# Optimization experiments

Hardware: AMD Instinct MI355X
Metric: run time of the kernel (lower is better)

## Reference

```python
import jax, jax.numpy as jnp
import numpy as np

NEG_SLOPE = 0.2  # PyG GATConv default negative_slope


def gat_conv(x, src, dst, W, a_src, a_dst, b):
    """PyG GATConv with concat=False (mean over heads). src/dst include self-loops."""
    N = x.shape[0]
    H, C = a_src.shape
    h = (x @ W).reshape(N, H, C)                      # [N,H,C]
    alpha_src = (h * a_src).sum(-1)                   # [N,H]
    alpha_dst = (h * a_dst).sum(-1)                   # [N,H]
    e = jax.nn.leaky_relu(alpha_src[src] + alpha_dst[dst], NEG_SLOPE)  # [E,H]
    # segment softmax over incoming edges of each dst node
    emax = jax.ops.segment_max(e, dst, num_segments=N)                 # [N,H]
    ex = jnp.exp(e - emax[dst])                                        # [E,H]
    denom = jax.ops.segment_sum(ex, dst, num_segments=N)               # [N,H]
    alpha = ex / denom[dst]                                            # [E,H]
    msg = h[src] * alpha[:, :, None]                                   # [E,H,C]
    out = jax.ops.segment_sum(msg, dst, num_segments=N)                # [N,H,C]
    return out.mean(axis=1) + b                                        # concat=False -> mean heads


def setup_inputs() -> dict:
    key = jax.random.key(0)
    ks = jax.random.split(key, 16)
    N, F_IN, H, C, E = 50000, 3, 4, 64, 800000
    inp = {
        "x": jax.random.normal(ks[0], (N, F_IN), dtype=jnp.float32),
        "edge_index": jax.random.randint(ks[1], (2, E), 0, N, dtype=jnp.int32),
        "W1": jax.random.normal(ks[2], (F_IN, H * C), dtype=jnp.float32) * 0.1,
        "a1_src": jax.random.normal(ks[3], (H, C), dtype=jnp.float32) * 0.1,
        "a1_dst": jax.random.normal(ks[4], (H, C), dtype=jnp.float32) * 0.1,
        "b1": jnp.zeros((C,), dtype=jnp.float32),
        "W2": jax.random.normal(ks[5], (C, H * C), dtype=jnp.float32) * 0.1,
        "a2_src": jax.random.normal(ks[6], (H, C), dtype=jnp.float32) * 0.1,
        "a2_dst": jax.random.normal(ks[7], (H, C), dtype=jnp.float32) * 0.1,
        "b2": jnp.zeros((C,), dtype=jnp.float32),
        "W3": jax.random.normal(ks[8], (C, H * C), dtype=jnp.float32) * 0.1,
        "a3_src": jax.random.normal(ks[9], (H, C), dtype=jnp.float32) * 0.1,
        "a3_dst": jax.random.normal(ks[10], (H, C), dtype=jnp.float32) * 0.1,
        "b3": jnp.zeros((C,), dtype=jnp.float32),
        "lin_w": jax.random.normal(ks[11], (C, 1), dtype=jnp.float32) * 0.1,
        "lin_b": jnp.zeros((1,), dtype=jnp.float32),
    }
    return inp


def reference(x, edge_index, W1, a1_src, a1_dst, b1, W2, a2_src, a2_dst, b2,
              W3, a3_src, a3_dst, b3, lin_w, lin_b):
    N = x.shape[0]
    loops = jnp.arange(N, dtype=edge_index.dtype)  # PyG add_self_loops=True default
    src = jnp.concatenate([edge_index[0], loops])
    dst = jnp.concatenate([edge_index[1], loops])

    h1 = jax.nn.elu(gat_conv(x, src, dst, W1, a1_src, a1_dst, b1))
    h2 = jax.nn.elu(gat_conv(h1, src, dst, W2, a2_src, a2_dst, b2)) + h1
    h3 = jax.nn.elu(gat_conv(h2, src, dst, W3, a3_src, a3_dst, b3)) + h2
    return h3 @ lin_w + lin_b
```

## Files before the change

kernel.cpp:

```cpp
#include <hip/hip_runtime.h>
#include <math.h>

#define HEADS 4
#define CH 64
#define HC 256

typedef __attribute__((ext_vector_type(8))) short bf16x8;
typedef __attribute__((ext_vector_type(4))) float f32x4;

__device__ __forceinline__ float lrelu(float v) { return v > 0.f ? v : 0.2f * v; }

__device__ __forceinline__ unsigned int f2bf(float f) {
    unsigned int u = __float_as_uint(f);
    u += 0x7fffu + ((u >> 16) & 1u);
    return u >> 16;
}
__device__ __forceinline__ float bf2f(unsigned short u) {
    return __uint_as_float(((unsigned int)u) << 16);
}

__device__ __forceinline__ float4 wave_sum4(float4 v) {
#pragma unroll
    for (int m = 32; m; m >>= 1) {
        v.x += __shfl_xor(v.x, m);
        v.y += __shfl_xor(v.y, m);
        v.z += __shfl_xor(v.z, m);
        v.w += __shfl_xor(v.w, m);
    }
    return v;
}

__global__ void count_kernel(const int* __restrict__ dst, int E, int vec_ok,
                             float scale8, int* __restrict__ deg,
                             int* __restrict__ slot) {
    int r = blockIdx.x & 7;
    int i = (blockIdx.x >> 3) * blockDim.x + threadIdx.x;
    int e0 = i * 4;
    if (e0 >= E) return;
    int d[4];
    int cnt;
    if (vec_ok && e0 + 3 < E) {
        int4 v = *(const int4*)(dst + e0);
        d[0] = v.x; d[1] = v.y; d[2] = v.z; d[3] = v.w; cnt = 4;
    } else {
        cnt = min(4, E - e0);
        for (int k = 0; k < cnt; ++k) d[k] = dst[e0 + k];
    }
    for (int k = 0; k < cnt; ++k) {
        int rr = min(7, (int)((float)d[k] * scale8));
        if (rr == r) slot[e0 + k] = atomicAdd(&deg[d[k]], 1);
    }
}

__global__ void scan_blocks(const int* __restrict__ deg,
                            int* __restrict__ off,
                            int* __restrict__ bsum,
                            const float* __restrict__ x,
                            float4* __restrict__ xq, int N) {
    __shared__ int sh[256];
    int t = threadIdx.x;
    int g = blockIdx.x * 256 + t;
    int v = (g < N) ? deg[g] + 1 : 0;
    if (g < N) xq[g] = make_float4(x[3 * g], x[3 * g + 1], x[3 * g + 2], 0.f);
    sh[t] = v;
    __syncthreads();
    for (int d = 1; d < 256; d <<= 1) {
        int xv = (t >= d) ? sh[t - d] : 0;
        __syncthreads();
        sh[t] += xv;
        __syncthreads();
    }
    if (g < N) off[g] = sh[t] - v;
    if (t == 255) bsum[blockIdx.x] = sh[255];
}

__global__ void scan_bsums(int* __restrict__ bsum, int G,
                           int* __restrict__ total_out) {
    __shared__ int sh[256];
    int t = threadIdx.x;
    int chunk = (G + 255) / 256;
    int lo = t * chunk, hi = min(lo + chunk, G);
    int s = 0;
    for (int i = lo; i < hi; ++i) s += bsum[i];
    sh[t] = s;
    __syncthreads();
    for (int d = 1; d < 256; d <<= 1) {
        int xv = (t >= d) ? sh[t - d] : 0;
        __syncthreads();
        sh[t] += xv;
        __syncthreads();
    }
    int run = (t > 0) ? sh[t - 1] : 0;
    for (int i = lo; i < hi; ++i) { int v = bsum[i]; bsum[i] = run; run += v; }
    if (t == 255) *total_out = sh[255];
}

__global__ void scan_add(int* __restrict__ off, const int* __restrict__ bsum,
                         const int* __restrict__ deg,
                         int* __restrict__ csr_src, int N) {
    int g = blockIdx.x * 256 + threadIdx.x;
    if (g < N) {
        int o = off[g] + bsum[blockIdx.x];
        off[g] = o;
        csr_src[o + deg[g]] = g;
    }
}

__global__ void scatter_plain(const int* __restrict__ src,
                              const int* __restrict__ dst,
                              const int* __restrict__ slot, int E, int vec_ok,
                              const int* __restrict__ off,
                              int* __restrict__ csr_src) {
    int i = blockIdx.x * blockDim.x + threadIdx.x;
    int e0 = i * 4;
    if (e0 >= E) return;
    if (vec_ok && e0 + 3 < E) {
        int4 sv = *(const int4*)(src + e0);
        int4 dv = *(const int4*)(dst + e0);
        int4 pv = *(const int4*)(slot + e0);
        csr_src[off[dv.x] + pv.x] = sv.x;
        csr_src[off[dv.y] + pv.y] = sv.y;
        csr_src[off[dv.z] + pv.z] = sv.z;
        csr_src[off[dv.w] + pv.w] = sv.w;
    } else {
        int cnt = min(4, E - e0);
        for (int k = 0; k < cnt; ++k) {
            int e = e0 + k;
            csr_src[off[dst[e]] + slot[e]] = src[e];
        }
    }
}

__device__ __forceinline__ void prep_blk(int b, int t, const float* W,
                                         const float* a_s, const float* a_d,
                                         unsigned short* Wb, float* ws,
                                         float* wd) {
    if (b < 64) {
        Wb[b * 256 + t] = (unsigned short)f2bf(W[(t >> 2) * HC + (t & 3) * CH + b]);
    } else {
        int idx = (b - 64) * 256 + t;
        int which = idx >= 256;
        int i = which ? idx - 256 : idx;
        int k = i >> 2, h = i & 3;
        const float* av = (which ? a_d : a_s) + h * CH;
        const float* Wr = W + (size_t)k * HC + h * CH;
        float s = 0.f;
        for (int c = 0; c < CH; ++c) s += Wr[c] * av[c];
        (which ? wd : ws)[i] = s;
    }
}

__global__ void prep_all(const float* __restrict__ W1,
                         const float* __restrict__ a1s,
                         const float* __restrict__ a1d,
                         float* __restrict__ ws1, float* __restrict__ wd1,
                         const float* __restrict__ W2,
                         const float* __restrict__ a2s,
                         const float* __restrict__ a2d,
                         unsigned short* __restrict__ Wb2,
                         float* __restrict__ ws2, float* __restrict__ wd2,
                         const float* __restrict__ W3,
                         const float* __restrict__ a3s,
                         const float* __restrict__ a3d,
                         unsigned short* __restrict__ Wb3,
                         float* __restrict__ ws3, float* __restrict__ wd3) {
    int b = blockIdx.x, t = threadIdx.x;
    if (b < 66) {
        prep_blk(b, t, W2, a2s, a2d, Wb2, ws2, wd2);
    } else if (b < 132) {
        prep_blk(b - 66, t, W3, a3s, a3d, Wb3, ws3, wd3);
    } else {
        for (int idx = t; idx < 24; idx += blockDim.x) {
            int which = idx >= 12;
            int i = which ? idx - 12 : idx;
            int k = i >> 2, h = i & 3;
            const float* av = (which ? a1d : a1s) + h * CH;
            const float* Wr = W1 + (size_t)k * HC + h * CH;
            float s = 0.f;
            for (int c = 0; c < CH; ++c) s += Wr[c] * av[c];
            (which ? wd1 : ws1)[i] = s;
        }
    }
}

__global__ void agg_kernel(const int* __restrict__ off,
                           const int* __restrict__ csr_src,
                           const unsigned short* __restrict__ xp,
                           const float4* __restrict__ asrc4,
                           const float4* __restrict__ adst4,
                           unsigned short* __restrict__ zb, int N) {
    __shared__ float4 exs[4][64];
    __shared__ unsigned int sss[4][64];
    int node = (blockIdx.x * blockDim.x + threadIdx.x) >> 6;
    int w = (threadIdx.x >> 6) & 3;
    int lane = threadIdx.x & 63;
    if (node >= N) return;
    int half = lane >> 5;
    int lk = lane & 31;
    int o0 = off[node], o1 = off[node + 1];
    int deg = o1 - o0;
    float4 ad = adst4[node];

    float l0 = 0.f, l1 = 0.f, l2 = 0.f, l3 = 0.f;
    float z[8];
#pragma unroll
    for (int q = 0; q < 8; ++q) z[q] = 0.f;
    const char* xpb2 = (const char*)xp + lk * 4;

    for (int base = 0; base < deg; base += 64) {
        int i = base + lane;
        int s = 0;
        float4 ev = make_float4(-INFINITY, -INFINITY, -INFINITY, -INFINITY);
        if (i < deg) {
            s = csr_src[o0 + i];
            float4 as = asrc4[s];
            ev.x = lrelu(as.x + ad.x);
            ev.y = lrelu(as.y + ad.y);
            ev.z = lrelu(as.z + ad.z);
            ev.w = lrelu(as.w + ad.w);
        }
        float4 ex;
        ex.x = __expf(ev.x);
        ex.y = __expf(ev.y);
        ex.z = __expf(ev.z);
        ex.w = __expf(ev.w);
        float4 ls = wave_sum4(ex);
        l0 += ls.x; l1 += ls.y; l2 += ls.z; l3 += ls.w;
        exs[w][lane] = ex;
        sss[w][lane] = (unsigned)s * 128u;

        int cnt = min(64, deg - base);
#pragma unroll 2
        for (int e2 = 0; e2 < cnt; e2 += 2) {
            int e = e2 + half;
            unsigned soff = sss[w][e];
            float4 exe = exs[w][e];
            unsigned xx = *(const unsigned*)(xpb2 + soff);
            float xk0 = bf2f((unsigned short)(xx & 0xffffu));
            float xk1 = bf2f((unsigned short)(xx >> 16));
            z[0] += exe.x * xk0; z[1] += exe.y * xk0;
            z[2] += exe.z * xk0; z[3] += exe.w * xk0;
            z[4] += exe.x * xk1; z[5] += exe.y * xk1;
            z[6] += exe.z * xk1; z[7] += exe.w * xk1;
        }
    }
#pragma unroll
    for (int q = 0; q < 8; ++q) z[q] += __shfl_xor(z[q], 32);

    float s0 = 0.25f / l0, s1 = 0.25f / l1, s2 = 0.25f / l2, s3 = 0.25f / l3;
    if (half == 0) {
        uint4 zo;
        zo.x = f2bf(z[0] * s0) | (f2bf(z[1] * s1) << 16);
        zo.y = f2bf(z[2] * s2) | (f2bf(z[3] * s3) << 16);
        zo.z = f2bf(z[4] * s0) | (f2bf(z[5] * s1) << 16);
        zo.w = f2bf(z[6] * s2) | (f2bf(z[7] * s3) << 16);
        *(uint4*)((char*)zb + (size_t)node * 512 + lk * 16) = zo;
    }
}

__global__ void gemm_mfma(const unsigned short* __restrict__ zb,
                          const unsigned short* __restrict__ Wb,
                          const float* __restrict__ bias,
                          const float* __restrict__ residual,
                          const float4* __restrict__ wsn4,
                          const float4* __restrict__ wdn4,
                          float4* __restrict__ asrc4,
                          float4* __restrict__ adst4,
                          const float* __restrict__ lin_w,
                          const float* __restrict__ lin_b,
                          float* __restrict__ out_f32,
                          unsigned short* __restrict__ out_pack,
                          float* __restrict__ out_final, int N) {
    int w = threadIdx.x >> 6;
    int lane = threadIdx.x & 63;
    int quad = lane >> 4, col = lane & 15;
    int nbase = blockIdx.x * 64 + w * 16;

    f32x4 zero4 = {0.f, 0.f, 0.f, 0.f};
    f32x4 acc[4];
#pragma unroll
    for (int t = 0; t < 4; ++t) acc[t] = zero4;

    const unsigned short* arow = zb + (size_t)(nbase + col) * HC + quad * 8;
#pragma unroll
    for (int q = 0; q < 8; ++q) {
        bf16x8 af = *(const bf16x8*)(arow + q * 32);
#pragma unroll
        for (int t = 0; t < 4; ++t) {
            const unsigned short* bp = Wb + (size_t)(t * 16 + col) * HC + q * 32 + quad * 8;
            bf16x8 bfrag = *(const bf16x8*)bp;
            acc[t] = __builtin_amdgcn_mfma_f32_16x16x32_bf16(af, bfrag, acc[t], 0, 0, 0);
        }
    }

    if (!out_final) {
        float vv[4][4];
#pragma unroll
        for (int t = 0; t < 4; ++t) {
            int c = t * 16 + col;
            float bc = bias[c];
#pragma unroll
            for (int r = 0; r < 4; ++r) {
                int n = nbase + quad * 4 + r;
                float v = acc[t][r] + bc;
                v = v > 0.f ? v : expm1f(v);
                v += residual[(size_t)n * CH + c];
                vv[t][r] = v;
                if (n < N) {
                    out_f32[(size_t)n * CH + c] = v;
                    out_pack[(size_t)n * CH + c] = (unsigned short)f2bf(v);
                }
            }
        }
        float4 wsv[4], wdv[4];
#pragma unroll
        for (int t = 0; t < 4; ++t) { wsv[t] = wsn4[t * 16 + col]; wdv[t] = wdn4[t * 16 + col]; }
#pragma unroll
        for (int r = 0; r < 4; ++r) {
            int n = nbase + quad * 4 + r;
            float4 sa = make_float4(0.f, 0.f, 0.f, 0.f);
            float4 da = make_float4(0.f, 0.f, 0.f, 0.f);
#pragma unroll
            for (int t = 0; t < 4; ++t) {
                float v = vv[t][r];
                sa.x += v * wsv[t].x; sa.y += v * wsv[t].y;
                sa.z += v * wsv[t].z; sa.w += v * wsv[t].w;
                da.x += v * wdv[t].x; da.y += v * wdv[t].y;
                da.z += v * wdv[t].z; da.w += v * wdv[t].w;
            }
#pragma unroll
            for (int m = 8; m; m >>= 1) {
                sa.x += __shfl_xor(sa.x, m); sa.y += __shfl_xor(sa.y, m);
                sa.z += __shfl_xor(sa.z, m); sa.w += __shfl_xor(sa.w, m);
                da.x += __shfl_xor(da.x, m); da.y += __shfl_xor(da.y, m);
                da.z += __shfl_xor(da.z, m); da.w += __shfl_xor(da.w, m);
            }
            if (col == 0 && n < N) { asrc4[n] = sa; adst4[n] = da; }
        }
    } else {
        float lw[4], bb[4];
#pragma unroll
        for (int t = 0; t < 4; ++t) { lw[t] = lin_w[t * 16 + col]; bb[t] = bias[t * 16 + col]; }
#pragma unroll
        for (int r = 0; r < 4; ++r) {
            int n = nbase + quad * 4 + r;
            float ts = 0.f;
#pragma unroll
            for (int t = 0; t < 4; ++t) {
                float v = acc[t][r] + bb[t];
                v = v > 0.f ? v : expm1f(v);
                v += residual[(size_t)n * CH + (t * 16 + col)];
                ts += v * lw[t];
            }
            ts += __shfl_xor(ts, 1);
            ts += __shfl_xor(ts, 2);
            ts += __shfl_xor(ts, 4);
            ts += __shfl_xor(ts, 8);
            if (col == 0 && n < N) out_final[n] = ts + lin_b[0];
        }
    }
}

__global__ void fused1_kernel(const int* __restrict__ off,
                              const int* __restrict__ csr_src,
                              const float4* __restrict__ xq,
                              const float* __restrict__ ws,
                              const float* __restrict__ wd,
                              float4* __restrict__ zl, int N) {
    int t = blockIdx.x * blockDim.x + threadIdx.x;
    int n = t >> 2, j = t & 3;
    if (n >= N) return;
    float4 xn = xq[n];
    float ad0 = xn.x * wd[0] + xn.y * wd[4] + xn.z * wd[8];
    float ad1 = xn.x * wd[1] + xn.y * wd[5] + xn.z * wd[9];
    float ad2 = xn.x * wd[2] + xn.y * wd[6] + xn.z * wd[10];
    float ad3 = xn.x * wd[3] + xn.y * wd[7] + xn.z * wd[11];

    int o0 = off[n], o1 = off[n + 1];
    float z[12];
#pragma unroll
    for (int q = 0; q < 12; ++q) z[q] = 0.f;
    float l0 = 0.f, l1 = 0.f, l2 = 0.f, l3 = 0.f;

    for (int i = o0 + j; i < o1; i += 4) {
        int s = csr_src[i];
        float4 xv = xq[s];
        float e0 = __expf(lrelu(xv.x * ws[0] + xv.y * ws[4] + xv.z * ws[8]  + ad0));
        float e1 = __expf(lrelu(xv.x * ws[1] + xv.y * ws[5] + xv.z * ws[9]  + ad1));
        float e2 = __expf(lrelu(xv.x * ws[2] + xv.y * ws[6] + xv.z * ws[10] + ad2));
        float e3 = __expf(lrelu(xv.x * ws[3] + xv.y * ws[7] + xv.z * ws[11] + ad3));
        l0 += e0; l1 += e1; l2 += e2; l3 += e3;
        z[0] += e0 * xv.x; z[1]  += e0 * xv.y; z[2]  += e0 * xv.z;
        z[3] += e1 * xv.x; z[4]  += e1 * xv.y; z[5]  += e1 * xv.z;
        z[6] += e2 * xv.x; z[7]  += e2 * xv.y; z[8]  += e2 * xv.z;
        z[9] += e3 * xv.x; z[10] += e3 * xv.y; z[11] += e3 * xv.z;
    }
#pragma unroll
    for (int m = 1; m < 4; m <<= 1) {
#pragma unroll
        for (int q = 0; q < 12; ++q) z[q] += __shfl_xor(z[q], m);
        l0 += __shfl_xor(l0, m);
        l1 += __shfl_xor(l1, m);
        l2 += __shfl_xor(l2, m);
        l3 += __shfl_xor(l3, m);
    }
    if (j == 0) {
        zl[(size_t)n * 4 + 0] = make_float4(z[0], z[1], z[2], z[3]);
        zl[(size_t)n * 4 + 1] = make_float4(z[4], z[5], z[6], z[7]);
        zl[(size_t)n * 4 + 2] = make_float4(z[8], z[9], z[10], z[11]);
        zl[(size_t)n * 4 + 3] = make_float4(l0, l1, l2, l3);
    }
}

__global__ void epi1_kernel(const float4* __restrict__ zl,
                            const float* __restrict__ W1,
                            const float* __restrict__ b1,
                            const float4* __restrict__ ws2_4,
                            const float4* __restrict__ wd2_4,
                            float4* __restrict__ asrc4,
                            float4* __restrict__ adst4,
                            float* __restrict__ out,
                            unsigned short* __restrict__ out_pack, int N) {
    int node = (blockIdx.x * blockDim.x + threadIdx.x) >> 6;
    int c = threadIdx.x & 63;
    if (node >= N) return;
    float4 z0 = zl[(size_t)node * 4 + 0];
    float4 z1 = zl[(size_t)node * 4 + 1];
    float4 z2 = zl[(size_t)node * 4 + 2];
    float4 l4 = zl[(size_t)node * 4 + 3];
    float i0 = 0.25f / l4.x, i1 = 0.25f / l4.y;
    float i2 = 0.25f / l4.z, i3 = 0.25f / l4.w;
    float acc =
        (z0.x * W1[0 * HC +   0 + c] + z0.y * W1[1 * HC +   0 + c] + z0.z * W1[2 * HC +   0 + c]) * i0 +
        (z0.w * W1[0 * HC +  64 + c] + z1.x * W1[1 * HC +  64 + c] + z1.y * W1[2 * HC +  64 + c]) * i1 +
        (z1.z * W1[0 * HC + 128 + c] + z1.w * W1[1 * HC + 128 + c] + z2.x * W1[2 * HC + 128 + c]) * i2 +
        (z2.y * W1[0 * HC + 192 + c] + z2.z * W1[1 * HC + 192 + c] + z2.w * W1[2 * HC + 192 + c]) * i3;
    float v = acc + b1[c];
    v = v > 0.f ? v : expm1f(v);
    out[(size_t)node * CH + c] = v;
    out_pack[(size_t)node * CH + c] = (unsigned short)f2bf(v);
    float4 wsv = ws2_4[c], wdv = wd2_4[c];
    float4 sacc = make_float4(v * wsv.x, v * wsv.y, v * wsv.z, v * wsv.w);
    float4 dacc = make_float4(v * wdv.x, v * wdv.y, v * wdv.z, v * wdv.w);
    sacc = wave_sum4(sacc);
    dacc = wave_sum4(dacc);
    if (c == 0) { asrc4[node] = sacc; adst4[node] = dacc; }
}

extern "C" void kernel_launch(void* const* d_in, const int* in_sizes, int n_in,
                              void* d_out, int out_size, void* d_ws, size_t ws_size,
                              hipStream_t stream) {
    const float* x      = (const float*)d_in[0];
    const int*   ei     = (const int*)  d_in[1];
    const float* W1     = (const float*)d_in[2];
    const float* a1s    = (const float*)d_in[3];
    const float* a1d    = (const float*)d_in[4];
    const float* b1     = (const float*)d_in[5];
    const float* W2     = (const float*)d_in[6];
    const float* a2s    = (const float*)d_in[7];
    const float* a2d    = (const float*)d_in[8];
    const float* b2     = (const float*)d_in[9];
    const float* W3     = (const float*)d_in[10];
    const float* a3s    = (const float*)d_in[11];
    const float* a3d    = (const float*)d_in[12];
    const float* b3     = (const float*)d_in[13];
    const float* lin_w  = (const float*)d_in[14];
    const float* lin_b  = (const float*)d_in[15];

    const int N = in_sizes[0] / 3;
    const int E = in_sizes[1] / 2;
    const int Et = E + N;
    const int* src = ei;
    const int* dst = ei + E;
    const float scale8 = 8.0f / (float)N;
    const int vec_ok = ((((size_t)src | (size_t)dst) & 15) == 0) ? 1 : 0;

    float* xq_f   = (float*)d_ws;
    unsigned short* zb  = (unsigned short*)(xq_f + (size_t)N * 4);
    unsigned short* xpA = zb  + (size_t)N * HC;
    unsigned short* xpB = xpA + (size_t)N * CH;
    unsigned short* Wb2 = xpB + (size_t)N * CH;
    unsigned short* Wb3 = Wb2 + 16384;
    float* bufA   = (float*)(Wb3 + 16384);
    float* bufB   = bufA + (size_t)N * CH;
    float* zl     = bufB + (size_t)N * CH;
    float* asrc   = zl   + (size_t)N * 16;
    float* adst   = asrc + (size_t)N * 4;
    float* ws1    = adst + (size_t)N * 4;
    float* wd1    = ws1 + 16;
    float* ws2    = wd1 + 16;
    float* wd2    = ws2 + 256;
    float* ws3    = wd2 + 256;
    float* wd3    = ws3 + 256;
    int* deg      = (int*)(wd3 + 256);
    int* off      = deg + N;
    int* bsum     = off + N + 4;
    int* slot     = bsum + 256;
    int* csr_src  = slot + E;

    const int B = 256;
    const int G = (N + 255) / 256;
    const int EB4 = (E + 3) / 4;
    const int CB = (EB4 + B - 1) / B;

    hipMemsetAsync(deg, 0, (size_t)N * sizeof(int), stream);
    count_kernel<<<CB * 8, B, 0, stream>>>(dst, E, vec_ok, scale8, deg, slot);
    scan_blocks<<<G, B, 0, stream>>>(deg, off, bsum, x, (float4*)xq_f, N);
    scan_bsums<<<1, B, 0, stream>>>(bsum, G, off + N);
    scan_add<<<G, B, 0, stream>>>(off, bsum, deg, csr_src, N);
    scatter_plain<<<CB, B, 0, stream>>>(src, dst, slot, E, vec_ok, off, csr_src);

    prep_all<<<133, B, 0, stream>>>(W1, a1s, a1d, ws1, wd1,
                                    W2, a2s, a2d, Wb2, ws2, wd2,
                                    W3, a3s, a3d, Wb3, ws3, wd3);

    int nwave_blocks = (N * 64 + B - 1) / B;
    int ngemm_blocks = (N + 63) / 64;

    fused1_kernel<<<(N * 4 + B - 1) / B, B, 0, stream>>>(
        off, csr_src, (const float4*)xq_f, ws1, wd1, (float4*)zl, N);
    epi1_kernel<<<nwave_blocks, B, 0, stream>>>(
        (const float4*)zl, W1, b1, (const float4*)ws2, (const float4*)wd2,
        (float4*)asrc, (float4*)adst, bufA, xpA, N);

    agg_kernel<<<nwave_blocks, B, 0, stream>>>(
        off, csr_src, xpA, (const float4*)asrc, (const float4*)adst,
        zb, N);
    gemm_mfma<<<ngemm_blocks, B, 0, stream>>>(
        zb, Wb2, b2, bufA, (const float4*)ws3, (const float4*)wd3,
        (float4*)asrc, (float4*)adst,
        nullptr, nullptr, bufB, xpB, nullptr, N);

    agg_kernel<<<nwave_blocks, B, 0, stream>>>(
        off, csr_src, xpB, (const float4*)asrc, (const float4*)adst,
        zb, N);
    gemm_mfma<<<ngemm_blocks, B, 0, stream>>>(
        zb, Wb3, b3, bufB, nullptr, nullptr, nullptr, nullptr,
        lin_w, lin_b, nullptr, nullptr, (float*)d_out, N);
}
```

Before: 319.8 us.

## Fuse scan, scatter/prep and layer-1 kernels to cut launches

```diff
diff --git a/kernel.cpp b/kernel.cpp
--- a/kernel.cpp
+++ b/kernel.cpp
@@ -74,60 +74,27 @@
     if (t == 255) bsum[blockIdx.x] = sh[255];
 }
 
-__global__ void scan_bsums(int* __restrict__ bsum, int G,
-                           int* __restrict__ total_out) {
-    __shared__ int sh[256];
-    int t = threadIdx.x;
-    int chunk = (G + 255) / 256;
-    int lo = t * chunk, hi = min(lo + chunk, G);
-    int s = 0;
-    for (int i = lo; i < hi; ++i) s += bsum[i];
-    sh[t] = s;
-    __syncthreads();
-    for (int d = 1; d < 256; d <<= 1) {
-        int xv = (t >= d) ? sh[t - d] : 0;
-        __syncthreads();
-        sh[t] += xv;
-        __syncthreads();
-    }
-    int run = (t > 0) ? sh[t - 1] : 0;
-    for (int i = lo; i < hi; ++i) { int v = bsum[i]; bsum[i] = run; run += v; }
-    if (t == 255) *total_out = sh[255];
-}
-
 __global__ void scan_add(int* __restrict__ off, const int* __restrict__ bsum,
                          const int* __restrict__ deg,
                          int* __restrict__ csr_src, int N) {
-    int g = blockIdx.x * 256 + threadIdx.x;
+    __shared__ int sh[256];
+    int t = threadIdx.x, bid = blockIdx.x;
+    int s = 0;
+    for (int i = t; i < bid; i += 256) s += bsum[i];
+    sh[t] = s;
+    __syncthreads();
+    for (int d = 128; d > 0; d >>= 1) {
+        if (t < d) sh[t] += sh[t + d];
+        __syncthreads();
+    }
+    int base = sh[0];
+    int g = bid * 256 + t;
     if (g < N) {
-        int o = off[g] + bsum[blockIdx.x];
+        int o = off[g] + base;
         off[g] = o;
-        csr_src[o + deg[g]] = g;
-    }
-}
-
-__global__ void scatter_plain(const int* __restrict__ src,
-                              const int* __restrict__ dst,
-                              const int* __restrict__ slot, int E, int vec_ok,
-                              const int* __restrict__ off,
-                              int* __restrict__ csr_src) {
-    int i = blockIdx.x * blockDim.x + threadIdx.x;
-    int e0 = i * 4;
-    if (e0 >= E) return;
-    if (vec_ok && e0 + 3 < E) {
-        int4 sv = *(const int4*)(src + e0);
-        int4 dv = *(const int4*)(dst + e0);
-        int4 pv = *(const int4*)(slot + e0);
-        csr_src[off[dv.x] + pv.x] = sv.x;
-        csr_src[off[dv.y] + pv.y] = sv.y;
-        csr_src[off[dv.z] + pv.z] = sv.z;
-        csr_src[off[dv.w] + pv.w] = sv.w;
-    } else {
-        int cnt = min(4, E - e0);
-        for (int k = 0; k < cnt; ++k) {
-            int e = e0 + k;
-            csr_src[off[dst[e]] + slot[e]] = src[e];
-        }
+        int dg = deg[g];
+        csr_src[o + dg] = g;
+        if (g == N - 1) off[N] = o + dg + 1;
     }
 }
 
@@ -150,21 +117,48 @@
     }
 }
 
-__global__ void prep_all(const float* __restrict__ W1,
-                         const float* __restrict__ a1s,
-                         const float* __restrict__ a1d,
-                         float* __restrict__ ws1, float* __restrict__ wd1,
-                         const float* __restrict__ W2,
-                         const float* __restrict__ a2s,
-                         const float* __restrict__ a2d,
-                         unsigned short* __restrict__ Wb2,
-                         float* __restrict__ ws2, float* __restrict__ wd2,
-                         const float* __restrict__ W3,
-                         const float* __restrict__ a3s,
-                         const float* __restrict__ a3d,
-                         unsigned short* __restrict__ Wb3,
-                         float* __restrict__ ws3, float* __restrict__ wd3) {
-    int b = blockIdx.x, t = threadIdx.x;
+__global__ void scatter_prep(const int* __restrict__ src,
+                             const int* __restrict__ dst,
+                             const int* __restrict__ slot, int E, int vec_ok,
+                             const int* __restrict__ off,
+                             int* __restrict__ csr_src, int CB,
+                             const float* __restrict__ W1,
+                             const float* __restrict__ a1s,
+                             const float* __restrict__ a1d,
+                             float* __restrict__ ws1, float* __restrict__ wd1,
+                             const float* __restrict__ W2,
+                             const float* __restrict__ a2s,
+                             const float* __restrict__ a2d,
+                             unsigned short* __restrict__ Wb2,
+                             float* __restrict__ ws2, float* __restrict__ wd2,
+                             const float* __restrict__ W3,
+                             const float* __restrict__ a3s,
+                             const float* __restrict__ a3d,
+                             unsigned short* __restrict__ Wb3,
+                             float* __restrict__ ws3, float* __restrict__ wd3) {
+    int bid = blockIdx.x;
+    int t = threadIdx.x;
+    if (bid < CB) {
+        int e0 = (bid * blockDim.x + t) * 4;
+        if (e0 >= E) return;
+        if (vec_ok && e0 + 3 < E) {
+            int4 sv = *(const int4*)(src + e0);
+            int4 dv = *(const int4*)(dst + e0);
+            int4 pv = *(const int4*)(slot + e0);
+            csr_src[off[dv.x] + pv.x] = sv.x;
+            csr_src[off[dv.y] + pv.y] = sv.y;
+            csr_src[off[dv.z] + pv.z] = sv.z;
+            csr_src[off[dv.w] + pv.w] = sv.w;
+        } else {
+            int cnt = min(4, E - e0);
+            for (int k = 0; k < cnt; ++k) {
+                int e = e0 + k;
+                csr_src[off[dst[e]] + slot[e]] = src[e];
+            }
+        }
+        return;
+    }
+    int b = bid - CB;
     if (b < 66) {
         prep_blk(b, t, W2, a2s, a2d, Wb2, ws2, wd2);
     } else if (b < 132) {
@@ -180,6 +174,97 @@
             for (int c = 0; c < CH; ++c) s += Wr[c] * av[c];
             (which ? wd1 : ws1)[i] = s;
         }
+    }
+}
+
+__global__ void l1_kernel(const int* __restrict__ off,
+                          const int* __restrict__ csr_src,
+                          const float4* __restrict__ xq,
+                          const float* __restrict__ ws,
+                          const float* __restrict__ wd,
+                          const float* __restrict__ W1,
+                          const float* __restrict__ b1,
+                          const float4* __restrict__ ws2_4,
+                          const float4* __restrict__ wd2_4,
+                          float4* __restrict__ asrc4,
+                          float4* __restrict__ adst4,
+                          float* __restrict__ out,
+                          unsigned short* __restrict__ out_pack, int N) {
+    __shared__ float zsh[64][16];
+    int t = threadIdx.x;
+    int ln = t >> 2, j = t & 3;
+    int node = blockIdx.x * 64 + ln;
+
+    if (node < N) {
+        float4 xn = xq[node];
+        float ad0 = xn.x * wd[0] + xn.y * wd[4] + xn.z * wd[8];
+        float ad1 = xn.x * wd[1] + xn.y * wd[5] + xn.z * wd[9];
+        float ad2 = xn.x * wd[2] + xn.y * wd[6] + xn.z * wd[10];
+        float ad3 = xn.x * wd[3] + xn.y * wd[7] + xn.z * wd[11];
+
+        int o0 = off[node], o1 = off[node + 1];
+        float z[12];
+#pragma unroll
+        for (int q = 0; q < 12; ++q) z[q] = 0.f;
+        float l0 = 0.f, l1 = 0.f, l2 = 0.f, l3 = 0.f;
+
+        for (int i = o0 + j; i < o1; i += 4) {
+            int s = csr_src[i];
+            float4 xv = xq[s];
+            float e0 = __expf(lrelu(xv.x * ws[0] + xv.y * ws[4] + xv.z * ws[8]  + ad0));
+            float e1 = __expf(lrelu(xv.x * ws[1] + xv.y * ws[5] + xv.z * ws[9]  + ad1));
+            float e2 = __expf(lrelu(xv.x * ws[2] + xv.y * ws[6] + xv.z * ws[10] + ad2));
+            float e3 = __expf(lrelu(xv.x * ws[3] + xv.y * ws[7] + xv.z * ws[11] + ad3));
+            l0 += e0; l1 += e1; l2 += e2; l3 += e3;
+            z[0] += e0 * xv.x; z[1]  += e0 * xv.y; z[2]  += e0 * xv.z;
+            z[3] += e1 * xv.x; z[4]  += e1 * xv.y; z[5]  += e1 * xv.z;
+            z[6] += e2 * xv.x; z[7]  += e2 * xv.y; z[8]  += e2 * xv.z;
+            z[9] += e3 * xv.x; z[10] += e3 * xv.y; z[11] += e3 * xv.z;
+        }
+#pragma unroll
+        for (int m = 1; m < 4; m <<= 1) {
+#pragma unroll
+            for (int q = 0; q < 12; ++q) z[q] += __shfl_xor(z[q], m);
+            l0 += __shfl_xor(l0, m);
+            l1 += __shfl_xor(l1, m);
+            l2 += __shfl_xor(l2, m);
+            l3 += __shfl_xor(l3, m);
+        }
+        float4 wv;
+        if (j == 0)      wv = make_float4(z[0], z[1], z[2],  z[3]);
+        else if (j == 1) wv = make_float4(z[4], z[5], z[6],  z[7]);
+        else if (j == 2) wv = make_float4(z[8], z[9], z[10], z[11]);
+        else             wv = make_float4(l0, l1, l2, l3);
+        *(float4*)&zsh[ln][j * 4] = wv;
+    }
+    __syncthreads();
+
+    int w = t >> 6, c = t & 63;
+    for (int ii = 0; ii < 16; ++ii) {
+        int ln2 = w * 16 + ii;
+        int n2 = blockIdx.x * 64 + ln2;
+        if (n2 >= N) break;
+        float4 z0 = *(const float4*)&zsh[ln2][0];
+        float4 z1 = *(const float4*)&zsh[ln2][4];
+        float4 z2 = *(const float4*)&zsh[ln2][8];
+        float4 l4 = *(const float4*)&zsh[ln2][12];
+        float i0 = 0.25f / l4.x, i1 = 0.25f / l4.y;
+        float i2 = 0.25f / l4.z, i3 = 0.25f / l4.w;
+        float acc =
+            (z0.x * W1[0 * HC +   0 + c] + z0.y * W1[1 * HC +   0 + c] + z0.z * W1[2 * HC +   0 + c]) * i0 +
+            (z0.w * W1[0 * HC +  64 + c] + z1.x * W1[1 * HC +  64 + c] + z1.y * W1[2 * HC +  64 + c]) * i1 +
+            (z1.z * W1[0 * HC + 128 + c] + z1.w * W1[1 * HC + 128 + c] + z2.x * W1[2 * HC + 128 + c]) * i2 +
+            (z2.y * W1[0 * HC + 192 + c] + z2.z * W1[1 * HC + 192 + c] + z2.w * W1[2 * HC + 192 + c]) * i3;
+        float v = acc + b1[c];
+        v = v > 0.f ? v : expm1f(v);
+        out[(size_t)n2 * CH + c] = v;
+        out_pack[(size_t)n2 * CH + c] = (unsigned short)f2bf(v);
+        float4 wsv = ws2_4[c], wdv = wd2_4[c];
+        float4 sacc = make_float4(v * wsv.x, v * wsv.y, v * wsv.z, v * wsv.w);
+        float4 dacc = make_float4(v * wdv.x, v * wdv.y, v * wdv.z, v * wdv.w);
+        sacc = wave_sum4(sacc);
+        dacc = wave_sum4(dacc);
+        if (c == 0) { asrc4[n2] = sacc; adst4[n2] = dacc; }
     }
 }
 
@@ -224,8 +309,6 @@
         ex.y = __expf(ev.y);
         ex.z = __expf(ev.z);
         ex.w = __expf(ev.w);
-        float4 ls = wave_sum4(ex);
-        l0 += ls.x; l1 += ls.y; l2 += ls.z; l3 += ls.w;
         exs[w][lane] = ex;
         sss[w][lane] = (unsigned)s * 128u;
 
@@ -235,6 +318,7 @@
             int e = e2 + half;
             unsigned soff = sss[w][e];
             float4 exe = exs[w][e];
+            l0 += exe.x; l1 += exe.y; l2 += exe.z; l3 += exe.w;
             unsigned xx = *(const unsigned*)(xpb2 + soff);
             float xk0 = bf2f((unsigned short)(xx & 0xffffu));
             float xk1 = bf2f((unsigned short)(xx >> 16));
@@ -246,6 +330,10 @@
     }
 #pragma unroll
     for (int q = 0; q < 8; ++q) z[q] += __shfl_xor(z[q], 32);
+    l0 += __shfl_xor(l0, 32);
+    l1 += __shfl_xor(l1, 32);
+    l2 += __shfl_xor(l2, 32);
+    l3 += __shfl_xor(l3, 32);
 
     float s0 = 0.25f / l0, s1 = 0.25f / l1, s2 = 0.25f / l2, s3 = 0.25f / l3;
     if (half == 0) {
@@ -359,92 +447,6 @@
             if (col == 0 && n < N) out_final[n] = ts + lin_b[0];
         }
     }
-}
-
-__global__ void fused1_kernel(const int* __restrict__ off,
-                              const int* __restrict__ csr_src,
-                              const float4* __restrict__ xq,
-                              const float* __restrict__ ws,
-                              const float* __restrict__ wd,
-                              float4* __restrict__ zl, int N) {
-    int t = blockIdx.x * blockDim.x + threadIdx.x;
-    int n = t >> 2, j = t & 3;
-    if (n >= N) return;
-    float4 xn = xq[n];
-    float ad0 = xn.x * wd[0] + xn.y * wd[4] + xn.z * wd[8];
-    float ad1 = xn.x * wd[1] + xn.y * wd[5] + xn.z * wd[9];
-    float ad2 = xn.x * wd[2] + xn.y * wd[6] + xn.z * wd[10];
-    float ad3 = xn.x * wd[3] + xn.y * wd[7] + xn.z * wd[11];
-
-    int o0 = off[n], o1 = off[n + 1];
-    float z[12];
-#pragma unroll
-    for (int q = 0; q < 12; ++q) z[q] = 0.f;
-    float l0 = 0.f, l1 = 0.f, l2 = 0.f, l3 = 0.f;
-
-    for (int i = o0 + j; i < o1; i += 4) {
-        int s = csr_src[i];
-        float4 xv = xq[s];
-        float e0 = __expf(lrelu(xv.x * ws[0] + xv.y * ws[4] + xv.z * ws[8]  + ad0));
-        float e1 = __expf(lrelu(xv.x * ws[1] + xv.y * ws[5] + xv.z * ws[9]  + ad1));
-        float e2 = __expf(lrelu(xv.x * ws[2] + xv.y * ws[6] + xv.z * ws[10] + ad2));
-        float e3 = __expf(lrelu(xv.x * ws[3] + xv.y * ws[7] + xv.z * ws[11] + ad3));
-        l0 += e0; l1 += e1; l2 += e2; l3 += e3;
-        z[0] += e0 * xv.x; z[1]  += e0 * xv.y; z[2]  += e0 * xv.z;
-        z[3] += e1 * xv.x; z[4]  += e1 * xv.y; z[5]  += e1 * xv.z;
-        z[6] += e2 * xv.x; z[7]  += e2 * xv.y; z[8]  += e2 * xv.z;
-        z[9] += e3 * xv.x; z[10] += e3 * xv.y; z[11] += e3 * xv.z;
-    }
-#pragma unroll
-    for (int m = 1; m < 4; m <<= 1) {
-#pragma unroll
-        for (int q = 0; q < 12; ++q) z[q] += __shfl_xor(z[q], m);
-        l0 += __shfl_xor(l0, m);
-        l1 += __shfl_xor(l1, m);
-        l2 += __shfl_xor(l2, m);
-        l3 += __shfl_xor(l3, m);
-    }
-    if (j == 0) {
-        zl[(size_t)n * 4 + 0] = make_float4(z[0], z[1], z[2], z[3]);
-        zl[(size_t)n * 4 + 1] = make_float4(z[4], z[5], z[6], z[7]);
-        zl[(size_t)n * 4 + 2] = make_float4(z[8], z[9], z[10], z[11]);
-        zl[(size_t)n * 4 + 3] = make_float4(l0, l1, l2, l3);
-    }
-}
-
-__global__ void epi1_kernel(const float4* __restrict__ zl,
-                            const float* __restrict__ W1,
-                            const float* __restrict__ b1,
-                            const float4* __restrict__ ws2_4,
-                            const float4* __restrict__ wd2_4,
-                            float4* __restrict__ asrc4,
-                            float4* __restrict__ adst4,
-                            float* __restrict__ out,
-                            unsigned short* __restrict__ out_pack, int N) {
-    int node = (blockIdx.x * blockDim.x + threadIdx.x) >> 6;
-    int c = threadIdx.x & 63;
-    if (node >= N) return;
-    float4 z0 = zl[(size_t)node * 4 + 0];
-    float4 z1 = zl[(size_t)node * 4 + 1];
-    float4 z2 = zl[(size_t)node * 4 + 2];
-    float4 l4 = zl[(size_t)node * 4 + 3];
-    float i0 = 0.25f / l4.x, i1 = 0.25f / l4.y;
-    float i2 = 0.25f / l4.z, i3 = 0.25f / l4.w;
-    float acc =
-        (z0.x * W1[0 * HC +   0 + c] + z0.y * W1[1 * HC +   0 + c] + z0.z * W1[2 * HC +   0 + c]) * i0 +
-        (z0.w * W1[0 * HC +  64 + c] + z1.x * W1[1 * HC +  64 + c] + z1.y * W1[2 * HC +  64 + c]) * i1 +
-        (z1.z * W1[0 * HC + 128 + c] + z1.w * W1[1 * HC + 128 + c] + z2.x * W1[2 * HC + 128 + c]) * i2 +
-        (z2.y * W1[0 * HC + 192 + c] + z2.z * W1[1 * HC + 192 + c] + z2.w * W1[2 * HC + 192 + c]) * i3;
-    float v = acc + b1[c];
-    v = v > 0.f ? v : expm1f(v);
-    out[(size_t)node * CH + c] = v;
-    out_pack[(size_t)node * CH + c] = (unsigned short)f2bf(v);
-    float4 wsv = ws2_4[c], wdv = wd2_4[c];
-    float4 sacc = make_float4(v * wsv.x, v * wsv.y, v * wsv.z, v * wsv.w);
-    float4 dacc = make_float4(v * wdv.x, v * wdv.y, v * wdv.z, v * wdv.w);
-    sacc = wave_sum4(sacc);
-    dacc = wave_sum4(dacc);
-    if (c == 0) { asrc4[node] = sacc; adst4[node] = dacc; }
 }
 
 extern "C" void kernel_launch(void* const* d_in, const int* in_sizes, int n_in,
@@ -483,8 +485,7 @@
     unsigned short* Wb3 = Wb2 + 16384;
     float* bufA   = (float*)(Wb3 + 16384);
     float* bufB   = bufA + (size_t)N * CH;
-    float* zl     = bufB + (size_t)N * CH;
-    float* asrc   = zl   + (size_t)N * 16;
+    float* asrc   = bufB + (size_t)N * CH;
     float* adst   = asrc + (size_t)N * 4;
     float* ws1    = adst + (size_t)N * 4;
     float* wd1    = ws1 + 16;
@@ -495,7 +496,7 @@
     int* deg      = (int*)(wd3 + 256);
     int* off      = deg + N;
     int* bsum     = off + N + 4;
-    int* slot     = bsum + 256;
+    int* slot     = bsum + 1024;
     int* csr_src  = slot + E;
 
     const int B = 256;
@@ -506,21 +507,19 @@
     hipMemsetAsync(deg, 0, (size_t)N * sizeof(int), stream);
     count_kernel<<<CB * 8, B, 0, stream>>>(dst, E, vec_ok, scale8, deg, slot);
     scan_blocks<<<G, B, 0, stream>>>(deg, off, bsum, x, (float4*)xq_f, N);
-    scan_bsums<<<1, B, 0, stream>>>(bsum, G, off + N);
     scan_add<<<G, B, 0, stream>>>(off, bsum, deg, csr_src, N);
-    scatter_plain<<<CB, B, 0, stream>>>(src, dst, slot, E, vec_ok, off, csr_src);
-
-    prep_all<<<133, B, 0, stream>>>(W1, a1s, a1d, ws1, wd1,
-                                    W2, a2s, a2d, Wb2, ws2, wd2,
-                                    W3, a3s, a3d, Wb3, ws3, wd3);
+    scatter_prep<<<CB + 133, B, 0, stream>>>(
+        src, dst, slot, E, vec_ok, off, csr_src, CB,
+        W1, a1s, a1d, ws1, wd1,
+        W2, a2s, a2d, Wb2, ws2, wd2,
+        W3, a3s, a3d, Wb3, ws3, wd3);
 
     int nwave_blocks = (N * 64 + B - 1) / B;
     int ngemm_blocks = (N + 63) / 64;
 
-    fused1_kernel<<<(N * 4 + B - 1) / B, B, 0, stream>>>(
-        off, csr_src, (const float4*)xq_f, ws1, wd1, (float4*)zl, N);
-    epi1_kernel<<<nwave_blocks, B, 0, stream>>>(
-        (const float4*)zl, W1, b1, (const float4*)ws2, (const float4*)wd2,
+    l1_kernel<<<ngemm_blocks, B, 0, stream>>>(
+        off, csr_src, (const float4*)xq_f, ws1, wd1, W1, b1,
+        (const float4*)ws2, (const float4*)wd2,
         (float4*)asrc, (float4*)adst, bufA, xpA, N);
 
     agg_kernel<<<nwave_blocks, B, 0, stream>>>(
```

After: 312.0 us. 1.02x faster.

## Fold block-sum scan into scan_add, merge scatter with prep, defer softmax denom reduction

Applied to the files above, without the earlier changes.

```diff
diff --git a/kernel.cpp b/kernel.cpp
--- a/kernel.cpp
+++ b/kernel.cpp
@@ -74,60 +74,27 @@
     if (t == 255) bsum[blockIdx.x] = sh[255];
 }
 
-__global__ void scan_bsums(int* __restrict__ bsum, int G,
-                           int* __restrict__ total_out) {
-    __shared__ int sh[256];
-    int t = threadIdx.x;
-    int chunk = (G + 255) / 256;
-    int lo = t * chunk, hi = min(lo + chunk, G);
-    int s = 0;
-    for (int i = lo; i < hi; ++i) s += bsum[i];
-    sh[t] = s;
-    __syncthreads();
-    for (int d = 1; d < 256; d <<= 1) {
-        int xv = (t >= d) ? sh[t - d] : 0;
-        __syncthreads();
-        sh[t] += xv;
-        __syncthreads();
-    }
-    int run = (t > 0) ? sh[t - 1] : 0;
-    for (int i = lo; i < hi; ++i) { int v = bsum[i]; bsum[i] = run; run += v; }
-    if (t == 255) *total_out = sh[255];
-}
-
 __global__ void scan_add(int* __restrict__ off, const int* __restrict__ bsum,
                          const int* __restrict__ deg,
                          int* __restrict__ csr_src, int N) {
-    int g = blockIdx.x * 256 + threadIdx.x;
+    __shared__ int sh[256];
+    int t = threadIdx.x, bid = blockIdx.x;
+    int s = 0;
+    for (int i = t; i < bid; i += 256) s += bsum[i];
+    sh[t] = s;
+    __syncthreads();
+    for (int d = 128; d > 0; d >>= 1) {
+        if (t < d) sh[t] += sh[t + d];
+        __syncthreads();
+    }
+    int base = sh[0];
+    int g = bid * 256 + t;
     if (g < N) {
-        int o = off[g] + bsum[blockIdx.x];
+        int o = off[g] + base;
         off[g] = o;
-        csr_src[o + deg[g]] = g;
-    }
-}
-
-__global__ void scatter_plain(const int* __restrict__ src,
-                              const int* __restrict__ dst,
-                              const int* __restrict__ slot, int E, int vec_ok,
-                              const int* __restrict__ off,
-                              int* __restrict__ csr_src) {
-    int i = blockIdx.x * blockDim.x + threadIdx.x;
-    int e0 = i * 4;
-    if (e0 >= E) return;
-    if (vec_ok && e0 + 3 < E) {
-        int4 sv = *(const int4*)(src + e0);
-        int4 dv = *(const int4*)(dst + e0);
-        int4 pv = *(const int4*)(slot + e0);
-        csr_src[off[dv.x] + pv.x] = sv.x;
-        csr_src[off[dv.y] + pv.y] = sv.y;
-        csr_src[off[dv.z] + pv.z] = sv.z;
-        csr_src[off[dv.w] + pv.w] = sv.w;
-    } else {
-        int cnt = min(4, E - e0);
-        for (int k = 0; k < cnt; ++k) {
-            int e = e0 + k;
-            csr_src[off[dst[e]] + slot[e]] = src[e];
-        }
+        int dg = deg[g];
+        csr_src[o + dg] = g;
+        if (g == N - 1) off[N] = o + dg + 1;
     }
 }
 
@@ -150,21 +117,48 @@
     }
 }
 
-__global__ void prep_all(const float* __restrict__ W1,
-                         const float* __restrict__ a1s,
-                         const float* __restrict__ a1d,
-                         float* __restrict__ ws1, float* __restrict__ wd1,
-                         const float* __restrict__ W2,
-                         const float* __restrict__ a2s,
-                         const float* __restrict__ a2d,
-                         unsigned short* __restrict__ Wb2,
-                         float* __restrict__ ws2, float* __restrict__ wd2,
-                         const float* __restrict__ W3,
-                         const float* __restrict__ a3s,
-                         const float* __restrict__ a3d,
-                         unsigned short* __restrict__ Wb3,
-                         float* __restrict__ ws3, float* __restrict__ wd3) {
-    int b = blockIdx.x, t = threadIdx.x;
+__global__ void scatter_prep(const int* __restrict__ src,
+                             const int* __restrict__ dst,
+                             const int* __restrict__ slot, int E, int vec_ok,
+                             const int* __restrict__ off,
+                             int* __restrict__ csr_src, int CB,
+                             const float* __restrict__ W1,
+                             const float* __restrict__ a1s,
+                             const float* __restrict__ a1d,
+                             float* __restrict__ ws1, float* __restrict__ wd1,
+                             const float* __restrict__ W2,
+                             const float* __restrict__ a2s,
+                             const float* __restrict__ a2d,
+                             unsigned short* __restrict__ Wb2,
+                             float* __restrict__ ws2, float* __restrict__ wd2,
+                             const float* __restrict__ W3,
+                             const float* __restrict__ a3s,
+                             const float* __restrict__ a3d,
+                             unsigned short* __restrict__ Wb3,
+                             float* __restrict__ ws3, float* __restrict__ wd3) {
+    int bid = blockIdx.x;
+    int t = threadIdx.x;
+    if (bid < CB) {
+        int e0 = (bid * blockDim.x + t) * 4;
+        if (e0 >= E) return;
+        if (vec_ok && e0 + 3 < E) {
+            int4 sv = *(const int4*)(src + e0);
+            int4 dv = *(const int4*)(dst + e0);
+            int4 pv = *(const int4*)(slot + e0);
+            csr_src[off[dv.x] + pv.x] = sv.x;
+            csr_src[off[dv.y] + pv.y] = sv.y;
+            csr_src[off[dv.z] + pv.z] = sv.z;
+            csr_src[off[dv.w] + pv.w] = sv.w;
+        } else {
+            int cnt = min(4, E - e0);
+            for (int k = 0; k < cnt; ++k) {
+                int e = e0 + k;
+                csr_src[off[dst[e]] + slot[e]] = src[e];
+            }
+        }
+        return;
+    }
+    int b = bid - CB;
     if (b < 66) {
         prep_blk(b, t, W2, a2s, a2d, Wb2, ws2, wd2);
     } else if (b < 132) {
@@ -179,184 +173,6 @@
             float s = 0.f;
             for (int c = 0; c < CH; ++c) s += Wr[c] * av[c];
             (which ? wd1 : ws1)[i] = s;
-        }
-    }
-}
-
-__global__ void agg_kernel(const int* __restrict__ off,
-                           const int* __restrict__ csr_src,
-                           const unsigned short* __restrict__ xp,
-                           const float4* __restrict__ asrc4,
-                           const float4* __restrict__ adst4,
-                           unsigned short* __restrict__ zb, int N) {
-    __shared__ float4 exs[4][64];
-    __shared__ unsigned int sss[4][64];
-    int node = (blockIdx.x * blockDim.x + threadIdx.x) >> 6;
-    int w = (threadIdx.x >> 6) & 3;
-    int lane = threadIdx.x & 63;
-    if (node >= N) return;
-    int half = lane >> 5;
-    int lk = lane & 31;
-    int o0 = off[node], o1 = off[node + 1];
-    int deg = o1 - o0;
-    float4 ad = adst4[node];
-
-    float l0 = 0.f, l1 = 0.f, l2 = 0.f, l3 = 0.f;
-    float z[8];
-#pragma unroll
-    for (int q = 0; q < 8; ++q) z[q] = 0.f;
-    const char* xpb2 = (const char*)xp + lk * 4;
-
-    for (int base = 0; base < deg; base += 64) {
-        int i = base + lane;
-        int s = 0;
-        float4 ev = make_float4(-INFINITY, -INFINITY, -INFINITY, -INFINITY);
-        if (i < deg) {
-            s = csr_src[o0 + i];
-            float4 as = asrc4[s];
-            ev.x = lrelu(as.x + ad.x);
-            ev.y = lrelu(as.y + ad.y);
-            ev.z = lrelu(as.z + ad.z);
-            ev.w = lrelu(as.w + ad.w);
-        }
-        float4 ex;
-        ex.x = __expf(ev.x);
-        ex.y = __expf(ev.y);
-        ex.z = __expf(ev.z);
-        ex.w = __expf(ev.w);
-        float4 ls = wave_sum4(ex);
-        l0 += ls.x; l1 += ls.y; l2 += ls.z; l3 += ls.w;
-        exs[w][lane] = ex;
-        sss[w][lane] = (unsigned)s * 128u;
-
-        int cnt = min(64, deg - base);
-#pragma unroll 2
-        for (int e2 = 0; e2 < cnt; e2 += 2) {
-            int e = e2 + half;
-            unsigned soff = sss[w][e];
-            float4 exe = exs[w][e];
-            unsigned xx = *(const unsigned*)(xpb2 + soff);
-            float xk0 = bf2f((unsigned short)(xx & 0xffffu));
-            float xk1 = bf2f((unsigned short)(xx >> 16));
-            z[0] += exe.x * xk0; z[1] += exe.y * xk0;
-            z[2] += exe.z * xk0; z[3] += exe.w * xk0;
-            z[4] += exe.x * xk1; z[5] += exe.y * xk1;
-            z[6] += exe.z * xk1; z[7] += exe.w * xk1;
-        }
-    }
-#pragma unroll
-    for (int q = 0; q < 8; ++q) z[q] += __shfl_xor(z[q], 32);
-
-    float s0 = 0.25f / l0, s1 = 0.25f / l1, s2 = 0.25f / l2, s3 = 0.25f / l3;
-    if (half == 0) {
-        uint4 zo;
-        zo.x = f2bf(z[0] * s0) | (f2bf(z[1] * s1) << 16);
-        zo.y = f2bf(z[2] * s2) | (f2bf(z[3] * s3) << 16);
-        zo.z = f2bf(z[4] * s0) | (f2bf(z[5] * s1) << 16);
-        zo.w = f2bf(z[6] * s2) | (f2bf(z[7] * s3) << 16);
-        *(uint4*)((char*)zb + (size_t)node * 512 + lk * 16) = zo;
-    }
-}
-
-__global__ void gemm_mfma(const unsigned short* __restrict__ zb,
-                          const unsigned short* __restrict__ Wb,
-                          const float* __restrict__ bias,
-                          const float* __restrict__ residual,
-                          const float4* __restrict__ wsn4,
-                          const float4* __restrict__ wdn4,
-                          float4* __restrict__ asrc4,
-                          float4* __restrict__ adst4,
-                          const float* __restrict__ lin_w,
-                          const float* __restrict__ lin_b,
-                          float* __restrict__ out_f32,
-                          unsigned short* __restrict__ out_pack,
-                          float* __restrict__ out_final, int N) {
-    int w = threadIdx.x >> 6;
-    int lane = threadIdx.x & 63;
-    int quad = lane >> 4, col = lane & 15;
-    int nbase = blockIdx.x * 64 + w * 16;
-
-    f32x4 zero4 = {0.f, 0.f, 0.f, 0.f};
-    f32x4 acc[4];
-#pragma unroll
-    for (int t = 0; t < 4; ++t) acc[t] = zero4;
-
-    const unsigned short* arow = zb + (size_t)(nbase + col) * HC + quad * 8;
-#pragma unroll
-    for (int q = 0; q < 8; ++q) {
-        bf16x8 af = *(const bf16x8*)(arow + q * 32);
-#pragma unroll
-        for (int t = 0; t < 4; ++t) {
-            const unsigned short* bp = Wb + (size_t)(t * 16 + col) * HC + q * 32 + quad * 8;
-            bf16x8 bfrag = *(const bf16x8*)bp;
-            acc[t] = __builtin_amdgcn_mfma_f32_16x16x32_bf16(af, bfrag, acc[t], 0, 0, 0);
-        }
-    }
-
-    if (!out_final) {
-        float vv[4][4];
-#pragma unroll
-        for (int t = 0; t < 4; ++t) {
-            int c = t * 16 + col;
-            float bc = bias[c];
-#pragma unroll
-            for (int r = 0; r < 4; ++r) {
-                int n = nbase + quad * 4 + r;
-                float v = acc[t][r] + bc;
-                v = v > 0.f ? v : expm1f(v);
-                v += residual[(size_t)n * CH + c];
-                vv[t][r] = v;
-                if (n < N) {
-                    out_f32[(size_t)n * CH + c] = v;
-                    out_pack[(size_t)n * CH + c] = (unsigned short)f2bf(v);
-                }
-            }
-        }
-        float4 wsv[4], wdv[4];
-#pragma unroll
-        for (int t = 0; t < 4; ++t) { wsv[t] = wsn4[t * 16 + col]; wdv[t] = wdn4[t * 16 + col]; }
-#pragma unroll
-        for (int r = 0; r < 4; ++r) {
-            int n = nbase + quad * 4 + r;
-            float4 sa = make_float4(0.f, 0.f, 0.f, 0.f);
-            float4 da = make_float4(0.f, 0.f, 0.f, 0.f);
-#pragma unroll
-            for (int t = 0; t < 4; ++t) {
-                float v = vv[t][r];
-                sa.x += v * wsv[t].x; sa.y += v * wsv[t].y;
-                sa.z += v * wsv[t].z; sa.w += v * wsv[t].w;
-                da.x += v * wdv[t].x; da.y += v * wdv[t].y;
-                da.z += v * wdv[t].z; da.w += v * wdv[t].w;
-            }
-#pragma unroll
-            for (int m = 8; m; m >>= 1) {
-                sa.x += __shfl_xor(sa.x, m); sa.y += __shfl_xor(sa.y, m);
-                sa.z += __shfl_xor(sa.z, m); sa.w += __shfl_xor(sa.w, m);
-                da.x += __shfl_xor(da.x, m); da.y += __shfl_xor(da.y, m);
-                da.z += __shfl_xor(da.z, m); da.w += __shfl_xor(da.w, m);
-            }
-            if (col == 0 && n < N) { asrc4[n] = sa; adst4[n] = da; }
-        }
-    } else {
-        float lw[4], bb[4];
-#pragma unroll
-        for (int t = 0; t < 4; ++t) { lw[t] = lin_w[t * 16 + col]; bb[t] = bias[t * 16 + col]; }
-#pragma unroll
-        for (int r = 0; r < 4; ++r) {
-            int n = nbase + quad * 4 + r;
-            float ts = 0.f;
-#pragma unroll
-            for (int t = 0; t < 4; ++t) {
-                float v = acc[t][r] + bb[t];
-                v = v > 0.f ? v : expm1f(v);
-                v += residual[(size_t)n * CH + (t * 16 + col)];
-                ts += v * lw[t];
-            }
-            ts += __shfl_xor(ts, 1);
-            ts += __shfl_xor(ts, 2);
-            ts += __shfl_xor(ts, 4);
-            ts += __shfl_xor(ts, 8);
-            if (col == 0 && n < N) out_final[n] = ts + lin_b[0];
         }
     }
 }
@@ -447,6 +263,187 @@
     if (c == 0) { asrc4[node] = sacc; adst4[node] = dacc; }
 }
 
+__global__ void agg_kernel(const int* __restrict__ off,
+                           const int* __restrict__ csr_src,
+                           const unsigned short* __restrict__ xp,
+                           const float4* __restrict__ asrc4,
+                           const float4* __restrict__ adst4,
+                           unsigned short* __restrict__ zb, int N) {
+    __shared__ float4 exs[4][64];
+    __shared__ unsigned int sss[4][64];
+    int node = (blockIdx.x * blockDim.x + threadIdx.x) >> 6;
+    int w = (threadIdx.x >> 6) & 3;
+    int lane = threadIdx.x & 63;
+    if (node >= N) return;
+    int half = lane >> 5;
+    int lk = lane & 31;
+    int o0 = off[node], o1 = off[node + 1];
+    int deg = o1 - o0;
+    float4 ad = adst4[node];
+
+    float l0 = 0.f, l1 = 0.f, l2 = 0.f, l3 = 0.f;
+    float z[8];
+#pragma unroll
+    for (int q = 0; q < 8; ++q) z[q] = 0.f;
+    const char* xpb2 = (const char*)xp + lk * 4;
+
+    for (int base = 0; base < deg; base += 64) {
+        int i = base + lane;
+        int s = 0;
+        float4 ev = make_float4(-INFINITY, -INFINITY, -INFINITY, -INFINITY);
+        if (i < deg) {
+            s = csr_src[o0 + i];
+            float4 as = asrc4[s];
+            ev.x = lrelu(as.x + ad.x);
+            ev.y = lrelu(as.y + ad.y);
+            ev.z = lrelu(as.z + ad.z);
+            ev.w = lrelu(as.w + ad.w);
+        }
+        float4 ex;
+        ex.x = __expf(ev.x);
+        ex.y = __expf(ev.y);
+        ex.z = __expf(ev.z);
+        ex.w = __expf(ev.w);
+        exs[w][lane] = ex;
+        sss[w][lane] = (unsigned)s * 128u;
+
+        int cnt = min(64, deg - base);
+#pragma unroll 2
+        for (int e2 = 0; e2 < cnt; e2 += 2) {
+            int e = e2 + half;
+            unsigned soff = sss[w][e];
+            float4 exe = exs[w][e];
+            l0 += exe.x; l1 += exe.y; l2 += exe.z; l3 += exe.w;
+            unsigned xx = *(const unsigned*)(xpb2 + soff);
+            float xk0 = bf2f((unsigned short)(xx & 0xffffu));
+            float xk1 = bf2f((unsigned short)(xx >> 16));
+            z[0] += exe.x * xk0; z[1] += exe.y * xk0;
+            z[2] += exe.z * xk0; z[3] += exe.w * xk0;
+            z[4] += exe.x * xk1; z[5] += exe.y * xk1;
+            z[6] += exe.z * xk1; z[7] += exe.w * xk1;
+        }
+    }
+#pragma unroll
+    for (int q = 0; q < 8; ++q) z[q] += __shfl_xor(z[q], 32);
+    l0 += __shfl_xor(l0, 32);
+    l1 += __shfl_xor(l1, 32);
+    l2 += __shfl_xor(l2, 32);
+    l3 += __shfl_xor(l3, 32);
+
+    float s0 = 0.25f / l0, s1 = 0.25f / l1, s2 = 0.25f / l2, s3 = 0.25f / l3;
+    if (half == 0) {
+        uint4 zo;
+        zo.x = f2bf(z[0] * s0) | (f2bf(z[1] * s1) << 16);
+        zo.y = f2bf(z[2] * s2) | (f2bf(z[3] * s3) << 16);
+        zo.z = f2bf(z[4] * s0) | (f2bf(z[5] * s1) << 16);
+        zo.w = f2bf(z[6] * s2) | (f2bf(z[7] * s3) << 16);
+        *(uint4*)((char*)zb + (size_t)node * 512 + lk * 16) = zo;
+    }
+}
+
+__global__ void gemm_mfma(const unsigned short* __restrict__ zb,
+                          const unsigned short* __restrict__ Wb,
+                          const float* __restrict__ bias,
+                          const float* __restrict__ residual,
+                          const float4* __restrict__ wsn4,
+                          const float4* __restrict__ wdn4,
+                          float4* __restrict__ asrc4,
+                          float4* __restrict__ adst4,
+                          const float* __restrict__ lin_w,
+                          const float* __restrict__ lin_b,
+                          float* __restrict__ out_f32,
+                          unsigned short* __restrict__ out_pack,
+                          float* __restrict__ out_final, int N) {
+    int w = threadIdx.x >> 6;
+    int lane = threadIdx.x & 63;
+    int quad = lane >> 4, col = lane & 15;
+    int nbase = blockIdx.x * 64 + w * 16;
+
+    f32x4 zero4 = {0.f, 0.f, 0.f, 0.f};
+    f32x4 acc[4];
+#pragma unroll
+    for (int t = 0; t < 4; ++t) acc[t] = zero4;
+
+    const unsigned short* arow = zb + (size_t)(nbase + col) * HC + quad * 8;
+#pragma unroll
+    for (int q = 0; q < 8; ++q) {
+        bf16x8 af = *(const bf16x8*)(arow + q * 32);
+#pragma unroll
+        for (int t = 0; t < 4; ++t) {
+            const unsigned short* bp = Wb + (size_t)(t * 16 + col) * HC + q * 32 + quad * 8;
+            bf16x8 bfrag = *(const bf16x8*)bp;
+            acc[t] = __builtin_amdgcn_mfma_f32_16x16x32_bf16(af, bfrag, acc[t], 0, 0, 0);
+        }
+    }
+
+    if (!out_final) {
+        float vv[4][4];
+#pragma unroll
+        for (int t = 0; t < 4; ++t) {
+            int c = t * 16 + col;
+            float bc = bias[c];
+#pragma unroll
+            for (int r = 0; r < 4; ++r) {
+                int n = nbase + quad * 4 + r;
+                float v = acc[t][r] + bc;
+                v = v > 0.f ? v : expm1f(v);
+                v += residual[(size_t)n * CH + c];
+                vv[t][r] = v;
+                if (n < N) {
+                    out_f32[(size_t)n * CH + c] = v;
+                    out_pack[(size_t)n * CH + c] = (unsigned short)f2bf(v);
+                }
+            }
+        }
+        float4 wsv[4], wdv[4];
+#pragma unroll
+        for (int t = 0; t < 4; ++t) { wsv[t] = wsn4[t * 16 + col]; wdv[t] = wdn4[t * 16 + col]; }
+#pragma unroll
+        for (int r = 0; r < 4; ++r) {
+            int n = nbase + quad * 4 + r;
+            float4 sa = make_float4(0.f, 0.f, 0.f, 0.f);
+            float4 da = make_float4(0.f, 0.f, 0.f, 0.f);
+#pragma unroll
+            for (int t = 0; t < 4; ++t) {
+                float v = vv[t][r];
+                sa.x += v * wsv[t].x; sa.y += v * wsv[t].y;
+                sa.z += v * wsv[t].z; sa.w += v * wsv[t].w;
+                da.x += v * wdv[t].x; da.y += v * wdv[t].y;
+                da.z += v * wdv[t].z; da.w += v * wdv[t].w;
+            }
+#pragma unroll
+            for (int m = 8; m; m >>= 1) {
+                sa.x += __shfl_xor(sa.x, m); sa.y += __shfl_xor(sa.y, m);
+                sa.z += __shfl_xor(sa.z, m); sa.w += __shfl_xor(sa.w, m);
+                da.x += __shfl_xor(da.x, m); da.y += __shfl_xor(da.y, m);
+                da.z += __shfl_xor(da.z, m); da.w += __shfl_xor(da.w, m);
+            }
+            if (col == 0 && n < N) { asrc4[n] = sa; adst4[n] = da; }
+        }
+    } else {
+        float lw[4], bb[4];
+#pragma unroll
+        for (int t = 0; t < 4; ++t) { lw[t] = lin_w[t * 16 + col]; bb[t] = bias[t * 16 + col]; }
+#pragma unroll
+        for (int r = 0; r < 4; ++r) {
+            int n = nbase + quad * 4 + r;
+            float ts = 0.f;
+#pragma unroll
+            for (int t = 0; t < 4; ++t) {
+                float v = acc[t][r] + bb[t];
+                v = v > 0.f ? v : expm1f(v);
+                v += residual[(size_t)n * CH + (t * 16 + col)];
+                ts += v * lw[t];
+            }
+            ts += __shfl_xor(ts, 1);
+            ts += __shfl_xor(ts, 2);
+            ts += __shfl_xor(ts, 4);
+            ts += __shfl_xor(ts, 8);
+            if (col == 0 && n < N) out_final[n] = ts + lin_b[0];
+        }
+    }
+}
+
 extern "C" void kernel_launch(void* const* d_in, const int* in_sizes, int n_in,
                               void* d_out, int out_size, void* d_ws, size_t ws_size,
                               hipStream_t stream) {
@@ -495,7 +492,7 @@
     int* deg      = (int*)(wd3 + 256);
     int* off      = deg + N;
     int* bsum     = off + N + 4;
-    int* slot     = bsum + 256;
+    int* slot     = bsum + 1024;
     int* csr_src  = slot + E;
 
     const int B = 256;
@@ -506,13 +503,12 @@
     hipMemsetAsync(deg, 0, (size_t)N * sizeof(int), stream);
     count_kernel<<<CB * 8, B, 0, stream>>>(dst, E, vec_ok, scale8, deg, slot);
     scan_blocks<<<G, B, 0, stream>>>(deg, off, bsum, x, (float4*)xq_f, N);
-    scan_bsums<<<1, B, 0, stream>>>(bsum, G, off + N);
     scan_add<<<G, B, 0, stream>>>(off, bsum, deg, csr_src, N);
-    scatter_plain<<<CB, B, 0, stream>>>(src, dst, slot, E, vec_ok, off, csr_src);
-
-    prep_all<<<133, B, 0, stream>>>(W1, a1s, a1d, ws1, wd1,
-                                    W2, a2s, a2d, Wb2, ws2, wd2,
-                                    W3, a3s, a3d, Wb3, ws3, wd3);
+    scatter_prep<<<CB + 133, B, 0, stream>>>(
+        src, dst, slot, E, vec_ok, off, csr_src, CB,
+        W1, a1s, a1d, ws1, wd1,
+        W2, a2s, a2d, Wb2, ws2, wd2,
+        W3, a3s, a3d, Wb3, ws3, wd3);
 
     int nwave_blocks = (N * 64 + B - 1) / B;
     int ngemm_blocks = (N + 63) / 64;
```

Result: faster. 303.3 us, median of 2 (-5.2%).
